# Kernel optimization log

Measured on AMD Instinct MI355X. Metric: run time of the kernel, lower is better.

## Reference

```python
import jax, jax.numpy as jnp
import numpy as np

N = 1_048_576  # total points across the ragged batch
D = 128        # feature dim
B = 16         # number of clouds in the batch


def setup_inputs() -> dict:
    key = jax.random.key(0)
    k_x, = jax.random.split(key, 1)
    # ragged lengths summing exactly to N (deterministic via numpy RNG)
    rng = np.random.default_rng(0)
    raw = rng.integers(low=N // (2 * B), high=(3 * N) // (2 * B), size=B)
    raw = np.maximum(raw, 1)
    lengths = (raw * (N / raw.sum())).astype(np.int64)
    lengths[-1] += N - lengths.sum()  # fix rounding so sum == N
    assert lengths.sum() == N and (lengths > 0).all()
    segment_ids = jnp.asarray(np.repeat(np.arange(B), lengths), dtype=jnp.int32)
    x = jax.random.normal(k_x, (N, D), dtype=jnp.float32)
    return {
        "x": x,
        "segment_ids": segment_ids,
        "lengths": jnp.asarray(lengths, dtype=jnp.int32),
    }


def reference(x, segment_ids, lengths):
    # Fused per-segment mean: one pass over x instead of B slice+reduce_mean calls.
    num_segments = lengths.shape[0]  # static B
    sums = jax.ops.segment_sum(x, segment_ids, num_segments=num_segments)  # [B, D]
    return sums / lengths[:, None].astype(x.dtype)
```

## Files before the change

kernel.cpp:

```cpp
#include <hip/hip_runtime.h>


#define SEG_D 128
#define SEG_D4 32
#define NSEG 16

__device__ __forceinline__ void acc4(float4& a, const float4 v) {
  a.x += v.x; a.y += v.y; a.z += v.z; a.w += v.w;
}

__global__ __launch_bounds__(256) void seg_partial_kernel(
    const float* __restrict__ x,
    const int* __restrict__ lengths,
    float* __restrict__ partial) {
  const int s  = blockIdx.y;
  const int bx = blockIdx.x;
  const int xb = gridDim.x;

  long long start = 0;
  int len = 0;
#pragma unroll
  for (int i = 0; i < NSEG; ++i) {
    const int l = lengths[i];
    if (i < s) start += l;
    if (i == s) len = l;
  }

  const int ro = threadIdx.x >> 5;
  const int c  = threadIdx.x & 31;

  const float4* __restrict__ x4 = (const float4*)x;

  float4 a0 = make_float4(0.f, 0.f, 0.f, 0.f);
  float4 a1 = a0, a2 = a0, a3 = a0;

  const long long step  = (long long)xb * 32;
  long long r = (long long)bx * 32 + ro;
  const float4* p = x4 + (start + r) * SEG_D4 + c;
  const long long pstep = step * SEG_D4;

  for (; r + 24 < len; r += step) {
    const float4 v0 = p[0];
    const float4 v1 = p[8  * SEG_D4];
    const float4 v2 = p[16 * SEG_D4];
    const float4 v3 = p[24 * SEG_D4];
    acc4(a0, v0); acc4(a1, v1); acc4(a2, v2); acc4(a3, v3);
    p += pstep;
  }
  if (r < len)      acc4(a0, p[0]);
  if (r + 8 < len)  acc4(a1, p[8  * SEG_D4]);
  if (r + 16 < len) acc4(a2, p[16 * SEG_D4]);

  acc4(a0, a1); acc4(a2, a3); acc4(a0, a2);

  __shared__ float4 red[256];
  red[threadIdx.x] = a0;
  __syncthreads();
  if (threadIdx.x < 32) {
    float4 sum = red[threadIdx.x];
#pragma unroll
    for (int i = 1; i < 8; ++i) acc4(sum, red[threadIdx.x + i * 32]);
    ((float4*)partial)[((long long)s * xb + bx) * SEG_D4 + threadIdx.x] = sum;
  }
}

__global__ __launch_bounds__(256) void seg_finish_kernel(
    const float* __restrict__ partial,
    const int* __restrict__ lengths,
    float* __restrict__ out,
    int xb) {
  const int s  = blockIdx.x;
  const int bo = threadIdx.x >> 5;
  const int c  = threadIdx.x & 31;

  const float4* p4 = (const float4*)partial + (long long)s * xb * SEG_D4 + c;
  float4 sum = make_float4(0.f, 0.f, 0.f, 0.f);
  for (int b = bo; b < xb; b += 8) {
    acc4(sum, p4[(long long)b * SEG_D4]);
  }

  __shared__ float4 red[256];
  red[threadIdx.x] = sum;
  __syncthreads();
  if (threadIdx.x < 32) {
    float4 t = red[threadIdx.x];
#pragma unroll
    for (int i = 1; i < 8; ++i) acc4(t, red[threadIdx.x + i * 32]);
    const float inv = 1.0f / (float)lengths[s];
    t.x *= inv; t.y *= inv; t.z *= inv; t.w *= inv;
    ((float4*)out)[s * SEG_D4 + threadIdx.x] = t;
  }
}

extern "C" void kernel_launch(void* const* d_in, const int* in_sizes, int n_in,
                              void* d_out, int out_size, void* d_ws, size_t ws_size,
                              hipStream_t stream) {
  const float* x       = (const float*)d_in[0];
  const int*   lengths = (const int*)d_in[2];
  float*       out     = (float*)d_out;
  float*       partial = (float*)d_ws;

  int xb = 128;
  const size_t need_per_xb = (size_t)NSEG * SEG_D * sizeof(float);
  while (xb > 1 && (size_t)xb * need_per_xb > ws_size) xb >>= 1;

  dim3 grid1(xb, NSEG);
  seg_partial_kernel<<<grid1, 256, 0, stream>>>(x, lengths, partial);
  seg_finish_kernel<<<NSEG, SEG_D * 2, 0, stream>>>(partial, lengths, out, xb);
}
```

Measured before the change: 683.9 us.

## Partition rows into fixed chunks with two-segment split per block

Replaces the per-segment grid (segments × 128 blocks) with a flat grid of 512-row chunks, each block streaming its contiguous chunk and accumulating into two partial sums split at the one segment boundary it may cross. The finish kernel then gathers the chunk partials that belong to each segment, plus the tail partial from a boundary-straddling chunk. This balances work across blocks regardless of ragged segment lengths and makes accesses fully contiguous, at the cost of a larger partial buffer (2048 blocks) and an assumption that no chunk spans more than two segments. The row count is inferred from in_sizes with a heuristic for bytes versus elements.

```diff
diff --git a/kernel.cpp b/kernel.cpp
--- a/kernel.cpp
+++ b/kernel.cpp
@@ -1,94 +1,109 @@
 #include <hip/hip_runtime.h>
 
 
-#define SEG_D 128
-#define SEG_D4 32
-#define NSEG 16
+#define SEG_D   128
+#define SEG_D4  32
+#define NSEG    16
+#define CROWS   512
 
 __device__ __forceinline__ void acc4(float4& a, const float4 v) {
   a.x += v.x; a.y += v.y; a.z += v.z; a.w += v.w;
 }
 
 __global__ __launch_bounds__(256) void seg_partial_kernel(
-    const float* __restrict__ x,
+    const float4* __restrict__ x4,
     const int* __restrict__ lengths,
-    float* __restrict__ partial) {
-  const int s  = blockIdx.y;
-  const int bx = blockIdx.x;
-  const int xb = gridDim.x;
+    float4* __restrict__ partial,
+    int nrows) {
+  const int b = blockIdx.x;
+  const int t = threadIdx.x;
+  const long long row_lo = (long long)b * CROWS;
+  long long row_hi = row_lo + CROWS;
+  if (row_hi > nrows) row_hi = nrows;
 
-  long long start = 0;
-  int len = 0;
-#pragma unroll
+  long long pre = 0, endA = 0;
   for (int i = 0; i < NSEG; ++i) {
-    const int l = lengths[i];
-    if (i < s) start += l;
-    if (i == s) len = l;
+    const long long l = lengths[i];
+    if (pre + l > row_lo) { endA = pre + l; break; }
+    pre += l;
   }
+  const long long split = endA < row_hi ? endA : row_hi;
 
-  const int ro = threadIdx.x >> 5;
-  const int c  = threadIdx.x & 31;
-
-  const float4* __restrict__ x4 = (const float4*)x;
+  const float4* __restrict__ base = x4 + row_lo * SEG_D4;
+  const int nf  = (int)((row_hi - row_lo) * SEG_D4);
+  const int sp4 = (int)((split - row_lo) * SEG_D4);
 
   float4 a0 = make_float4(0.f, 0.f, 0.f, 0.f);
   float4 a1 = a0, a2 = a0, a3 = a0;
+  float4 b0 = a0, b1 = a0, b2 = a0, b3 = a0;
 
-  const long long step  = (long long)xb * 32;
-  long long r = (long long)bx * 32 + ro;
-  const float4* p = x4 + (start + r) * SEG_D4 + c;
-  const long long pstep = step * SEG_D4;
+  int i = t;
+  for (; i + 768 < nf; i += 1024) {
+    const float4 v0 = base[i];
+    const float4 v1 = base[i + 256];
+    const float4 v2 = base[i + 512];
+    const float4 v3 = base[i + 768];
+    if (i       < sp4) acc4(a0, v0); else acc4(b0, v0);
+    if (i + 256 < sp4) acc4(a1, v1); else acc4(b1, v1);
+    if (i + 512 < sp4) acc4(a2, v2); else acc4(b2, v2);
+    if (i + 768 < sp4) acc4(a3, v3); else acc4(b3, v3);
+  }
+  for (; i < nf; i += 256) {
+    const float4 v = base[i];
+    if (i < sp4) acc4(a0, v); else acc4(b0, v);
+  }
+  acc4(a0, a1); acc4(a2, a3); acc4(a0, a2);
+  acc4(b0, b1); acc4(b2, b3); acc4(b0, b2);
 
-  for (; r + 24 < len; r += step) {
-    const float4 v0 = p[0];
-    const float4 v1 = p[8  * SEG_D4];
-    const float4 v2 = p[16 * SEG_D4];
-    const float4 v3 = p[24 * SEG_D4];
-    acc4(a0, v0); acc4(a1, v1); acc4(a2, v2); acc4(a3, v3);
-    p += pstep;
-  }
-  if (r < len)      acc4(a0, p[0]);
-  if (r + 8 < len)  acc4(a1, p[8  * SEG_D4]);
-  if (r + 16 < len) acc4(a2, p[16 * SEG_D4]);
-
-  acc4(a0, a1); acc4(a2, a3); acc4(a0, a2);
-
-  __shared__ float4 red[256];
-  red[threadIdx.x] = a0;
+  __shared__ float4 red[2][256];
+  red[0][t] = a0;
+  red[1][t] = b0;
   __syncthreads();
-  if (threadIdx.x < 32) {
-    float4 sum = red[threadIdx.x];
+  if (t < 64) {
+    const int which = t >> 5;
+    const int c     = t & 31;
+    float4 sum = red[which][c];
 #pragma unroll
-    for (int i = 1; i < 8; ++i) acc4(sum, red[threadIdx.x + i * 32]);
-    ((float4*)partial)[((long long)s * xb + bx) * SEG_D4 + threadIdx.x] = sum;
+    for (int k = 1; k < 8; ++k) acc4(sum, red[which][c + k * 32]);
+    partial[((long long)b * 2 + which) * SEG_D4 + c] = sum;
   }
 }
 
 __global__ __launch_bounds__(256) void seg_finish_kernel(
-    const float* __restrict__ partial,
+    const float4* __restrict__ partial,
     const int* __restrict__ lengths,
-    float* __restrict__ out,
-    int xb) {
-  const int s  = blockIdx.x;
-  const int bo = threadIdx.x >> 5;
-  const int c  = threadIdx.x & 31;
+    float4* __restrict__ out) {
+  const int s    = blockIdx.x;
+  const int slot = threadIdx.x >> 5;
+  const int c    = threadIdx.x & 31;
 
-  const float4* p4 = (const float4*)partial + (long long)s * xb * SEG_D4 + c;
+  long long pre = 0;
+  for (int i = 0; i < s; ++i) pre += lengths[i];
+  const long long len = lengths[s];
+  const long long end = pre + len;
+
+  const int bA_lo = (int)((pre + CROWS - 1) / CROWS);
+  const int bA_hi = (int)((end - 1) / CROWS);
+
   float4 sum = make_float4(0.f, 0.f, 0.f, 0.f);
-  for (int b = bo; b < xb; b += 8) {
-    acc4(sum, p4[(long long)b * SEG_D4]);
+  for (int b = bA_lo + slot; b <= bA_hi; b += 8)
+    acc4(sum, partial[((long long)b * 2) * SEG_D4 + c]);
+
+  if (slot == 0 && (pre % CROWS) != 0) {
+    const int bx = (int)(pre / CROWS);
+    acc4(sum, partial[((long long)bx * 2 + 1) * SEG_D4 + c]);
   }
 
   __shared__ float4 red[256];
   red[threadIdx.x] = sum;
   __syncthreads();
   if (threadIdx.x < 32) {
-    float4 t = red[threadIdx.x];
+    float4 tt = red[threadIdx.x];
 #pragma unroll
-    for (int i = 1; i < 8; ++i) acc4(t, red[threadIdx.x + i * 32]);
-    const float inv = 1.0f / (float)lengths[s];
-    t.x *= inv; t.y *= inv; t.z *= inv; t.w *= inv;
-    ((float4*)out)[s * SEG_D4 + threadIdx.x] = t;
+    for (int k = 1; k < 8; ++k) acc4(tt, red[threadIdx.x + k * 32]);
+    const float inv = 1.0f / (float)len;
+    tt.x *= inv; tt.y *= inv; tt.z *= inv; tt.w *= inv;
+    out[s * SEG_D4 + threadIdx.x] = tt;
   }
 }
 
@@ -98,13 +113,16 @@
   const float* x       = (const float*)d_in[0];
   const int*   lengths = (const int*)d_in[2];
   float*       out     = (float*)d_out;
-  float*       partial = (float*)d_ws;
 
-  int xb = 128;
-  const size_t need_per_xb = (size_t)NSEG * SEG_D * sizeof(float);
-  while (xb > 1 && (size_t)xb * need_per_xb > ws_size) xb >>= 1;
+  const bool sizes_in_bytes = (in_sizes[2] >= 64);
+  const long long denom = sizes_in_bytes ? (long long)SEG_D * 4 : (long long)SEG_D;
+  const int nrows = (int)((long long)in_sizes[0] / denom);
+  const int T     = (nrows + CROWS - 1) / CROWS;
 
-  dim3 grid1(xb, NSEG);
-  seg_partial_kernel<<<grid1, 256, 0, stream>>>(x, lengths, partial);
-  seg_finish_kernel<<<NSEG, SEG_D * 2, 0, stream>>>(partial, lengths, out, xb);
+  float4* partial = (float4*)d_ws;
+
+  seg_partial_kernel<<<T, 256, 0, stream>>>(
+      (const float4*)x, lengths, partial, nrows);
+  seg_finish_kernel<<<NSEG, 256, 0, stream>>>(
+      partial, lengths, (float4*)out);
 }
```

Result: no change. 680.8 us, median of 2 (-0.5%).
